# Performance work log

Measured on AMD Instinct MI355X. Metric: run time of the kernel, lower is better.

Reference implementation:

```python
import jax, jax.numpy as jnp
import numpy as np

EPS = 1e-6
B, T, E, H = 2, 512, 1024, 256
NUM_BLOCK = 12


def normalize(x):
    # RMS-style normalization over the feature dim (no learned affine)
    return x * jax.lax.rsqrt(jnp.mean(x * x, axis=-1, keepdims=True) + EPS)


def bar_quadratic_causal(a, b):
    # y_i = (1/i) * sum_{j<=i} relu(a_i + b_j)   (causal prefix mean of pairwise relation)
    # a, b: [B, T, H]
    Tn = a.shape[1]
    pair = jax.nn.relu(a[:, :, None, :] + b[:, None, :, :])  # [B, T(i), T(j), H]
    mask = jnp.tril(jnp.ones((Tn, Tn), dtype=a.dtype))        # causal j<=i
    s = jnp.einsum('bijh,ij->bih', pair, mask)
    counts = jnp.arange(1, Tn + 1, dtype=a.dtype)[None, :, None]
    return s / counts


def setup_inputs() -> dict:
    key = jax.random.key(0)
    k0, k1, k2, k3 = jax.random.split(key, 4)
    x = jax.random.normal(k0, (B, T, E), dtype=jnp.float32)
    w1 = jax.random.normal(k1, (E, H), dtype=jnp.float32) * 0.02
    b1 = jnp.zeros((H,), dtype=jnp.float32)
    w2 = jax.random.normal(k2, (E, H), dtype=jnp.float32) * 0.02
    b2 = jnp.zeros((H,), dtype=jnp.float32)
    w3 = jax.random.normal(k3, (H, E), dtype=jnp.float32) * (0.02 / np.sqrt(NUM_BLOCK))
    b3 = jnp.zeros((E,), dtype=jnp.float32)
    return {"x": x, "w1": w1, "b1": b1, "w2": w2, "b2": b2, "w3": w3, "b3": b3}


def reference(x, w1, b1, w2, b2, w3, b3):
    r = normalize(x)
    a = r @ w1 + b1
    b = r @ w2 + b2
    # PreNorm == 'approx': normalize a and b separately
    a = normalize(a)
    b = normalize(b)
    r = bar_quadratic_causal(a, b)
    # PostNorm == 'yes'
    r = normalize(r)
    r = r @ w3 + b3
    return x + r
```

## Files before the change

### kernel.cpp

```cpp
#include <hip/hip_runtime.h>

#define EPSF 1e-6f
#define Bsz 2
#define Tn  512
#define En  1024
#define Hn  256
#define Mtot (Bsz * Tn)
typedef unsigned short us_t;
typedef unsigned int   u32_t;

typedef __attribute__((ext_vector_type(8))) __fp16 f16x8;
typedef __attribute__((ext_vector_type(2))) __fp16 h2_t;
typedef __attribute__((ext_vector_type(8))) short  short8;
typedef __attribute__((ext_vector_type(4))) float  f32x4;
#define MFMA16(a, b, c) __builtin_amdgcn_mfma_f32_16x16x32_f16((a), (b), (c), 0, 0, 0)

__device__ __forceinline__ us_t f2h(float f) {
  __fp16 h = (__fp16)f;
  return __builtin_bit_cast(us_t, h);
}
__device__ __forceinline__ float h2f(us_t u) {
  return (float)__builtin_bit_cast(__fp16, u);
}
__device__ __forceinline__ uint2 pack4h(float a, float b, float c, float d) {
  uint2 r;
  r.x = (u32_t)f2h(a) | ((u32_t)f2h(b) << 16);
  r.y = (u32_t)f2h(c) | ((u32_t)f2h(d) << 16);
  return r;
}
__device__ __forceinline__ float block_reduce_sum_256(float v, float* smem) {
  #pragma unroll
  for (int off = 32; off > 0; off >>= 1) v += __shfl_down(v, off, 64);
  const int wave = threadIdx.x >> 6;
  if ((threadIdx.x & 63) == 0) smem[wave] = v;
  __syncthreads();
  float s = smem[0] + smem[1] + smem[2] + smem[3];
  __syncthreads();
  return s;
}

__global__ __launch_bounds__(256) void k_prep(
    const float* __restrict__ x,
    const float* __restrict__ w1, const float* __restrict__ w2,
    const float* __restrict__ w3,
    us_t* __restrict__ xb, float* __restrict__ rs,
    us_t* __restrict__ w1t, us_t* __restrict__ w2t, us_t* __restrict__ w3t)
{
  const int b = blockIdx.x, t = threadIdx.x;

  if (b < 256) {
    const int wid = t >> 6, lane = t & 63;
    const int q   = b >> 3;
    const int mt  = (b & 7) + 8 * (q & 7);
    const int row = 16 * mt + 4 * (q >> 3) + wid;
    const float4* xp = (const float4*)(x + (size_t)row * En);
    float4 v[4];
    #pragma unroll
    for (int i = 0; i < 4; ++i) v[i] = xp[lane + 64 * i];
    float ss = 0.f;
    #pragma unroll
    for (int i = 0; i < 4; ++i)
      ss += v[i].x*v[i].x + v[i].y*v[i].y + v[i].z*v[i].z + v[i].w*v[i].w;
    #pragma unroll
    for (int off = 32; off > 0; off >>= 1) ss += __shfl_xor(ss, off, 64);
    if (lane == 0) rs[row] = rsqrtf(ss * (1.0f / En) + EPSF);
    uint2* xo = (uint2*)(xb + (size_t)row * En);
    #pragma unroll
    for (int i = 0; i < 4; ++i)
      xo[lane + 64 * i] = pack4h(v[i].x, v[i].y, v[i].z, v[i].w);
    return;
  }

  __shared__ float ts[32][33];
  const int i = b - 256;
  const float* src; us_t* dst; int R, C, tr, tc;
  if (i < 256)      { src = w1; dst = w1t; R = 1024; C = 256;  tr = i >> 3;  tc = i & 7; }
  else if (i < 512) { int k = i - 256; src = w2; dst = w2t; R = 1024; C = 256; tr = k >> 3; tc = k & 7; }
  else              { int k = i - 512; src = w3; dst = w3t; R = 256; C = 1024; tr = k >> 5; tc = k & 31; }

  const int r = t >> 3, c4 = (t & 7) * 4;
  float4 v = *(const float4*)(src + (size_t)(tr * 32 + r) * C + tc * 32 + c4);
  ts[r][c4 + 0] = v.x; ts[r][c4 + 1] = v.y; ts[r][c4 + 2] = v.z; ts[r][c4 + 3] = v.w;
  __syncthreads();
  float o0 = ts[c4 + 0][r], o1 = ts[c4 + 1][r], o2 = ts[c4 + 2][r], o3 = ts[c4 + 3][r];
  *(uint2*)(dst + (size_t)(tc * 32 + r) * R + tr * 32 + c4) = pack4h(o0, o1, o2, o3);
}

__global__ __launch_bounds__(256, 4) void k_gemm(
    const us_t* __restrict__ xb,
    const us_t* __restrict__ w1t, const us_t* __restrict__ w2t,
    float* __restrict__ Praw)
{
  const int blk = blockIdx.x;
  const int mt = blk & 63, nt = blk >> 6;
  const int m0 = mt * 16, n0 = nt * 32;
  const int wid = threadIdx.x >> 6, lane = threadIdx.x & 63;
  const int lg = lane >> 4, lr = lane & 15;
  const int k0 = wid * 256;

  const us_t* ap = xb + (size_t)(m0 + lr) * En + k0 + lg * 8;
  const us_t* bbase = (n0 < Hn) ? (w1t + (size_t)n0 * En)
                                : (w2t + (size_t)(n0 - Hn) * En);
  const us_t* bp0 = bbase + (size_t)lr * En + k0 + lg * 8;
  const us_t* bp1 = bp0 + (size_t)16 * En;

  f16x8 a[8], b0[8], b1[8];
  #pragma unroll
  for (int s = 0; s < 8; ++s) a[s]  = *(const f16x8*)(ap  + s * 32);
  #pragma unroll
  for (int s = 0; s < 8; ++s) b0[s] = *(const f16x8*)(bp0 + s * 32);
  #pragma unroll
  for (int s = 0; s < 8; ++s) b1[s] = *(const f16x8*)(bp1 + s * 32);

  f32x4 acc0 = {0.f,0.f,0.f,0.f}, acc1 = acc0;
  #pragma unroll
  for (int s = 0; s < 8; ++s) {
    acc0 = MFMA16(a[s], b0[s], acc0);
    acc1 = MFMA16(a[s], b1[s], acc1);
  }

  __shared__ float cmb[4][16][32];
  #pragma unroll
  for (int i = 0; i < 4; ++i) {
    cmb[wid][lg * 4 + i][lr]      = acc0[i];
    cmb[wid][lg * 4 + i][16 + lr] = acc1[i];
  }
  __syncthreads();

  #pragma unroll
  for (int e = 0; e < 2; ++e) {
    const int idx = threadIdx.x + e * 256;
    const int row = idx >> 5, col = idx & 31;
    float s = cmb[0][row][col] + cmb[1][row][col]
            + cmb[2][row][col] + cmb[3][row][col];
    Praw[(size_t)(m0 + row) * 512 + n0 + col] = s;
  }
}

__global__ __launch_bounds__(256) void k_norm(
    const float* __restrict__ Praw, const float* __restrict__ rs,
    const float* __restrict__ b1, const float* __restrict__ b2,
    us_t* __restrict__ A, us_t* __restrict__ BmT)
{
  const int blk = blockIdx.x, t = threadIdx.x;
  const int wid = t >> 6, lane = t & 63;
  const int h0 = lane * 4;

  if (blk < 256) {
    const int mt = blk & 63, sub = blk >> 6;
    const int r  = 16 * mt + 4 * sub + wid;
    float4 d = *(const float4*)(Praw + (size_t)r * 512 + h0);
    const float s0 = rs[r];
    float4 bv = *(const float4*)(b1 + h0);
    float vx = d.x * s0 + bv.x, vy = d.y * s0 + bv.y;
    float vz = d.z * s0 + bv.z, vw = d.w * s0 + bv.w;

    float ss = vx*vx + vy*vy + vz*vz + vw*vw;
    #pragma unroll
    for (int o2 = 32; o2 > 0; o2 >>= 1) ss += __shfl_xor(ss, o2, 64);
    const float sc = rsqrtf(ss * (1.0f / Hn) + EPSF);
    *(uint2*)(A + (size_t)r * Hn + h0) = pack4h(vx*sc, vy*sc, vz*sc, vw*sc);
    return;
  }

  __shared__ us_t ls[4][256];
  const int m  = blk - 256;
  const int mt = m & 63, sub = m >> 6;
  const int r0 = 16 * mt + 4 * sub;
  const int r  = r0 + wid;

  float4 d = *(const float4*)(Praw + (size_t)r * 512 + Hn + h0);
  const float s0 = rs[r];
  float4 bv = *(const float4*)(b2 + h0);
  float vx = d.x * s0 + bv.x, vy = d.y * s0 + bv.y;
  float vz = d.z * s0 + bv.z, vw = d.w * s0 + bv.w;

  float ss = vx*vx + vy*vy + vz*vz + vw*vw;
  #pragma unroll
  for (int o2 = 32; o2 > 0; o2 >>= 1) ss += __shfl_xor(ss, o2, 64);
  const float sc = rsqrtf(ss * (1.0f / Hn) + EPSF);

  *(uint2*)&ls[wid][h0] = pack4h(vx*sc, vy*sc, vz*sc, vw*sc);
  __syncthreads();

  const int h = t;
  u32_t w0  = (u32_t)ls[0][h] | ((u32_t)ls[1][h] << 16);
  u32_t w1v = (u32_t)ls[2][h] | ((u32_t)ls[3][h] << 16);
  const int bb   = r0 >> 9;
  const int tcol = r0 & 511;
  *(uint2*)(BmT + (size_t)bb * Hn * Tn + (size_t)h * Tn + tcol) = make_uint2(w0, w1v);
}

#define JCHB 32
__global__ __launch_bounds__(256) void k_bar(
    const us_t* __restrict__ A, const us_t* __restrict__ BmT,
    us_t* __restrict__ Yb)
{
  const int raw = blockIdx.x;
  const int sel = (raw < 256) ? raw : (511 - raw);
  const int bb  = raw >> 8;
  const int i0  = sel * 2;
  const int h   = threadIdx.x;
  const size_t baseA = (size_t)bb * Tn * Hn;
  const us_t* __restrict__ bt = BmT + (size_t)bb * Hn * Tn + (size_t)h * Tn;

  const __fp16 a0h = __builtin_bit_cast(__fp16, A[baseA + (size_t)i0 * Hn + h]);
  const __fp16 a1h = __builtin_bit_cast(__fp16, A[baseA + (size_t)(i0 + 1) * Hn + h]);
  const float av0 = (float)a0h;
  const float av1 = (float)a1h;
  h2_t z2;  z2[0]  = (__fp16)0.f; z2[1]  = (__fp16)0.f;
  h2_t a02; a02[0] = a0h;         a02[1] = a0h;
  h2_t a12; a12[0] = a1h;         a12[1] = a1h;
  float sum0 = 0.f, sum1 = 0.f;

  const int nfull = i0 & ~(JCHB - 1);
  short8 c0[4], c1[4];

  #define LOADC(dst, jj) { _Pragma("unroll") \
    for (int q = 0; q < 4; ++q) dst[q] = *(const short8*)(bt + (jj) + q * 8); }
  #define PROCP(buf) { _Pragma("unroll") \
    for (int q = 0; q < 4; ++q) { \
      const h2_t* ph = (const h2_t*)&buf[q]; \
      h2_t p0 = z2, p1 = z2; \
      _Pragma("unroll") \
      for (int w2i = 0; w2i < 4; ++w2i) { \
        h2_t bv2 = ph[w2i]; \
        p0 += __builtin_elementwise_max(a02 + bv2, z2); \
        p1 += __builtin_elementwise_max(a12 + bv2, z2); \
      } \
      sum0 += (float)p0[0] + (float)p0[1]; \
      sum1 += (float)p1[0] + (float)p1[1]; } }

  if (nfull > 0) {
    LOADC(c0, 0);
    int j = 0;
    while (true) {
      const bool m1 = (j + JCHB     < nfull);
      const bool m2 = (j + 2 * JCHB < nfull);
      if (m1) LOADC(c1, j + JCHB);
      PROCP(c0);
      j += JCHB;
      if (!m1) break;
      if (m2) LOADC(c0, j + JCHB);
      PROCP(c1);
      j += JCHB;
      if (!m2) break;
    }
  }
  {
    short8 ct[4];
    LOADC(ct, nfull);
    const int lim = i0 - nfull;
    #pragma unroll
    for (int q = 0; q < 4; ++q)
      #pragma unroll
      for (int e = 0; e < 8; ++e) {
        const int jl = q * 8 + e;
        float bv = h2f((us_t)ct[q][e]);
        sum0 += (jl <= lim)     ? fmaxf(av0 + bv, 0.f) : 0.f;
        sum1 += (jl <= lim + 1) ? fmaxf(av1 + bv, 0.f) : 0.f;
      }
  }
  #undef LOADC
  #undef PROCP

  __shared__ float red[4];
  {
    float ss = block_reduce_sum_256(sum0 * sum0, red);
    float c  = (float)(i0 + 1);
    float sc = rsqrtf(ss * (1.0f / Hn) + EPSF * c * c);
    Yb[baseA + (size_t)i0 * Hn + h] = f2h(sum0 * sc);
  }
  {
    float ss = block_reduce_sum_256(sum1 * sum1, red);
    float c  = (float)(i0 + 2);
    float sc = rsqrtf(ss * (1.0f / Hn) + EPSF * c * c);
    Yb[baseA + (size_t)(i0 + 1) * Hn + h] = f2h(sum1 * sc);
  }
}

__global__ __launch_bounds__(256, 4) void k_out(
    const us_t* __restrict__ Yb, const us_t* __restrict__ w3t,
    const float* __restrict__ x, const float* __restrict__ b3,
    float* __restrict__ out)
{
  const int wid = threadIdx.x >> 6, lane = threadIdx.x & 63;
  const int wg = blockIdx.x * 4 + wid;
  const int nt = wg & 63, mt = wg >> 6;
  const int m0 = mt * 16, n0 = nt * 16;
  const int lg = lane >> 4, lr = lane & 15;

  const us_t* ap = Yb  + (size_t)(m0 + lr) * Hn + lg * 8;
  const us_t* bp = w3t + (size_t)(n0 + lr) * Hn + lg * 8;

  f16x8 a[8], b[8];
  #pragma unroll
  for (int s = 0; s < 8; ++s) a[s] = *(const f16x8*)(ap + s * 32);
  #pragma unroll
  for (int s = 0; s < 8; ++s) b[s] = *(const f16x8*)(bp + s * 32);

  f32x4 acc = {0.f,0.f,0.f,0.f};
  #pragma unroll
  for (int s = 0; s < 8; ++s) acc = MFMA16(a[s], b[s], acc);

  const int row = m0 + lg * 4;
  const int c = n0 + lr;
  const float bv = b3[c];
  #pragma unroll
  for (int i = 0; i < 4; ++i) {
    const size_t o = (size_t)(row + i) * En + c;
    out[o] = x[o] + acc[i] + bv;
  }
}

extern "C" void kernel_launch(void* const* d_in, const int* in_sizes, int n_in,
                              void* d_out, int out_size, void* d_ws, size_t ws_size,
                              hipStream_t stream) {
  const float* x  = (const float*)d_in[0];
  const float* w1 = (const float*)d_in[1];
  const float* b1 = (const float*)d_in[2];
  const float* w2 = (const float*)d_in[3];
  const float* b2 = (const float*)d_in[4];
  const float* w3 = (const float*)d_in[5];
  const float* b3 = (const float*)d_in[6];
  float* out = (float*)d_out;

  char* q = (char*)d_ws;
  float* Praw = (float*)q;  q += (size_t)Mtot * 512 * 4;
  us_t* xb    = (us_t*)q;   q += (size_t)Mtot * En * 2;
  us_t* w1t   = (us_t*)q;   q += (size_t)Hn * En * 2;
  us_t* w2t   = (us_t*)q;   q += (size_t)Hn * En * 2;
  us_t* w3t   = (us_t*)q;   q += (size_t)En * Hn * 2;
  us_t* A     = (us_t*)q;   q += (size_t)Mtot * Hn * 2;
  us_t* BmT   = (us_t*)q;   q += (size_t)Mtot * Hn * 2;
  us_t* Yb    = (us_t*)q;   q += (size_t)Mtot * Hn * 2;
  float* rs   = (float*)q;  q += (size_t)Mtot * 4;

  k_prep<<<1024, 256, 0, stream>>>(x, w1, w2, w3, xb, rs, w1t, w2t, w3t);
  k_gemm<<<1024, 256, 0, stream>>>(xb, w1t, w2t, Praw);
  k_norm<<<512,  256, 0, stream>>>(Praw, rs, b1, b2, A, BmT);
  k_bar <<<512,  256, 0, stream>>>(A, BmT, Yb);
  k_out <<<1024, 256, 0, stream>>>(Yb, w3t, x, b3, out);
}
```

Before: 46.67 us.

## Fuse input RMS-norm into GEMM prologue and row-norm into last-block epilogue

Each GEMM block now computes the RMS scale of its 16 input rows and stages the normalized fp16 rows in shared memory, so the separate xb conversion buffer and the rs array are gone. The k_norm launch is removed. A per-row-tile atomic ticket lets the last of the 16 column blocks for that tile normalize both projection outputs and write A and the transposed B. This cuts one launch and the intermediate traffic, at the cost of every block re-reading x from global memory, the larger shared-memory footprint lowering occupancy, and a serialized epilogue in the last block.

```diff
diff --git a/kernel.cpp b/kernel.cpp
--- a/kernel.cpp
+++ b/kernel.cpp
@@ -39,44 +39,20 @@
   return s;
 }
 
-__global__ __launch_bounds__(256) void k_prep(
-    const float* __restrict__ x,
+__global__ __launch_bounds__(256) void k_tr(
     const float* __restrict__ w1, const float* __restrict__ w2,
     const float* __restrict__ w3,
-    us_t* __restrict__ xb, float* __restrict__ rs,
-    us_t* __restrict__ w1t, us_t* __restrict__ w2t, us_t* __restrict__ w3t)
+    us_t* __restrict__ w1t, us_t* __restrict__ w2t, us_t* __restrict__ w3t,
+    int* __restrict__ ticket)
 {
   const int b = blockIdx.x, t = threadIdx.x;
-
-  if (b < 256) {
-    const int wid = t >> 6, lane = t & 63;
-    const int q   = b >> 3;
-    const int mt  = (b & 7) + 8 * (q & 7);
-    const int row = 16 * mt + 4 * (q >> 3) + wid;
-    const float4* xp = (const float4*)(x + (size_t)row * En);
-    float4 v[4];
-    #pragma unroll
-    for (int i = 0; i < 4; ++i) v[i] = xp[lane + 64 * i];
-    float ss = 0.f;
-    #pragma unroll
-    for (int i = 0; i < 4; ++i)
-      ss += v[i].x*v[i].x + v[i].y*v[i].y + v[i].z*v[i].z + v[i].w*v[i].w;
-    #pragma unroll
-    for (int off = 32; off > 0; off >>= 1) ss += __shfl_xor(ss, off, 64);
-    if (lane == 0) rs[row] = rsqrtf(ss * (1.0f / En) + EPSF);
-    uint2* xo = (uint2*)(xb + (size_t)row * En);
-    #pragma unroll
-    for (int i = 0; i < 4; ++i)
-      xo[lane + 64 * i] = pack4h(v[i].x, v[i].y, v[i].z, v[i].w);
-    return;
-  }
+  if (b == 0 && t < 64) ticket[t] = 0;
 
   __shared__ float ts[32][33];
-  const int i = b - 256;
   const float* src; us_t* dst; int R, C, tr, tc;
-  if (i < 256)      { src = w1; dst = w1t; R = 1024; C = 256;  tr = i >> 3;  tc = i & 7; }
-  else if (i < 512) { int k = i - 256; src = w2; dst = w2t; R = 1024; C = 256; tr = k >> 3; tc = k & 7; }
-  else              { int k = i - 512; src = w3; dst = w3t; R = 256; C = 1024; tr = k >> 5; tc = k & 31; }
+  if (b < 256)      { src = w1; dst = w1t; R = 1024; C = 256;  tr = b >> 3;  tc = b & 7; }
+  else if (b < 512) { int k = b - 256; src = w2; dst = w2t; R = 1024; C = 256; tr = k >> 3; tc = k & 7; }
+  else              { int k = b - 512; src = w3; dst = w3t; R = 256; C = 1024; tr = k >> 5; tc = k & 31; }
 
   const int r = t >> 3, c4 = (t & 7) * 4;
   float4 v = *(const float4*)(src + (size_t)(tr * 32 + r) * C + tc * 32 + c4);
@@ -87,108 +63,148 @@
 }
 
 __global__ __launch_bounds__(256, 4) void k_gemm(
-    const us_t* __restrict__ xb,
+    const float* __restrict__ x,
     const us_t* __restrict__ w1t, const us_t* __restrict__ w2t,
-    float* __restrict__ Praw)
+    const float* __restrict__ b1, const float* __restrict__ b2,
+    float* __restrict__ Praw, int* __restrict__ ticket,
+    us_t* __restrict__ A, us_t* __restrict__ BmT)
 {
+  union SM {
+    us_t xs[16][1032];
+    struct { float cmb[4][16][32]; us_t ls[16][256]; } ep;
+  };
+  __shared__ SM sm;
+  __shared__ int winf;
+
   const int blk = blockIdx.x;
   const int mt = blk & 63, nt = blk >> 6;
   const int m0 = mt * 16, n0 = nt * 32;
-  const int wid = threadIdx.x >> 6, lane = threadIdx.x & 63;
+  const int t = threadIdx.x;
+
+  {
+    const int r  = t >> 4;
+    const int cs = t & 15;
+    const float* xr = x + (size_t)(m0 + r) * En;
+    float ss = 0.f;
+    #pragma unroll
+    for (int i = 0; i < 16; ++i) {
+      float4 v = *(const float4*)(xr + i * 64 + cs * 4);
+      ss += v.x*v.x + v.y*v.y + v.z*v.z + v.w*v.w;
+    }
+    #pragma unroll
+    for (int o = 1; o < 16; o <<= 1) ss += __shfl_xor(ss, o, 64);
+    const float sc = rsqrtf(ss * (1.0f / En) + EPSF);
+    #pragma unroll
+    for (int i = 0; i < 16; ++i) {
+      float4 v = *(const float4*)(xr + i * 64 + cs * 4);
+      *(uint2*)&sm.xs[r][i * 64 + cs * 4] =
+          pack4h(v.x * sc, v.y * sc, v.z * sc, v.w * sc);
+    }
+  }
+  __syncthreads();
+
+  const int wid = t >> 6, lane = t & 63;
   const int lg = lane >> 4, lr = lane & 15;
   const int k0 = wid * 256;
 
-  const us_t* ap = xb + (size_t)(m0 + lr) * En + k0 + lg * 8;
   const us_t* bbase = (n0 < Hn) ? (w1t + (size_t)n0 * En)
                                 : (w2t + (size_t)(n0 - Hn) * En);
   const us_t* bp0 = bbase + (size_t)lr * En + k0 + lg * 8;
   const us_t* bp1 = bp0 + (size_t)16 * En;
 
-  f16x8 a[8], b0[8], b1[8];
-  #pragma unroll
-  for (int s = 0; s < 8; ++s) a[s]  = *(const f16x8*)(ap  + s * 32);
-  #pragma unroll
-  for (int s = 0; s < 8; ++s) b0[s] = *(const f16x8*)(bp0 + s * 32);
-  #pragma unroll
-  for (int s = 0; s < 8; ++s) b1[s] = *(const f16x8*)(bp1 + s * 32);
+  f16x8 wf0[8], wf1[8];
+  #pragma unroll
+  for (int s = 0; s < 8; ++s) wf0[s] = *(const f16x8*)(bp0 + s * 32);
+  #pragma unroll
+  for (int s = 0; s < 8; ++s) wf1[s] = *(const f16x8*)(bp1 + s * 32);
 
   f32x4 acc0 = {0.f,0.f,0.f,0.f}, acc1 = acc0;
   #pragma unroll
   for (int s = 0; s < 8; ++s) {
-    acc0 = MFMA16(a[s], b0[s], acc0);
-    acc1 = MFMA16(a[s], b1[s], acc1);
-  }
-
-  __shared__ float cmb[4][16][32];
+    f16x8 a = *(const f16x8*)&sm.xs[lr][k0 + lg * 8 + s * 32];
+    acc0 = MFMA16(a, wf0[s], acc0);
+    acc1 = MFMA16(a, wf1[s], acc1);
+  }
+  __syncthreads();
+
   #pragma unroll
   for (int i = 0; i < 4; ++i) {
-    cmb[wid][lg * 4 + i][lr]      = acc0[i];
-    cmb[wid][lg * 4 + i][16 + lr] = acc1[i];
-  }
-  __syncthreads();
-
+    sm.ep.cmb[wid][lg * 4 + i][lr]      = acc0[i];
+    sm.ep.cmb[wid][lg * 4 + i][16 + lr] = acc1[i];
+  }
+  __syncthreads();
   #pragma unroll
   for (int e = 0; e < 2; ++e) {
-    const int idx = threadIdx.x + e * 256;
+    const int idx = t + e * 256;
     const int row = idx >> 5, col = idx & 31;
-    float s = cmb[0][row][col] + cmb[1][row][col]
-            + cmb[2][row][col] + cmb[3][row][col];
+    float s = sm.ep.cmb[0][row][col] + sm.ep.cmb[1][row][col]
+            + sm.ep.cmb[2][row][col] + sm.ep.cmb[3][row][col];
     Praw[(size_t)(m0 + row) * 512 + n0 + col] = s;
   }
-}
-
-__global__ __launch_bounds__(256) void k_norm(
-    const float* __restrict__ Praw, const float* __restrict__ rs,
-    const float* __restrict__ b1, const float* __restrict__ b2,
-    us_t* __restrict__ A, us_t* __restrict__ BmT)
-{
-  const int blk = blockIdx.x, t = threadIdx.x;
-  const int wid = t >> 6, lane = t & 63;
-  const int h0 = lane * 4;
-
-  if (blk < 256) {
-    const int mt = blk & 63, sub = blk >> 6;
-    const int r  = 16 * mt + 4 * sub + wid;
-    float4 d = *(const float4*)(Praw + (size_t)r * 512 + h0);
-    const float s0 = rs[r];
-    float4 bv = *(const float4*)(b1 + h0);
-    float vx = d.x * s0 + bv.x, vy = d.y * s0 + bv.y;
-    float vz = d.z * s0 + bv.z, vw = d.w * s0 + bv.w;
-
-    float ss = vx*vx + vy*vy + vz*vz + vw*vw;
-    #pragma unroll
-    for (int o2 = 32; o2 > 0; o2 >>= 1) ss += __shfl_xor(ss, o2, 64);
+
+  __threadfence();
+  __syncthreads();
+  if (t == 0) winf = (atomicAdd(&ticket[mt], 1) == 15);
+  __syncthreads();
+  if (!winf) return;
+
+  const int r  = t >> 4;
+  const int cs = t & 15;
+  const float* pr = Praw + (size_t)(m0 + r) * 512;
+
+  {
+    float v[16]; float ss = 0.f;
+    #pragma unroll
+    for (int q = 0; q < 4; ++q) {
+      float4 d  = *(const float4*)(pr + cs * 16 + q * 4);
+      float4 bv = *(const float4*)(b1 + cs * 16 + q * 4);
+      v[q*4+0] = d.x + bv.x; v[q*4+1] = d.y + bv.y;
+      v[q*4+2] = d.z + bv.z; v[q*4+3] = d.w + bv.w;
+    }
+    #pragma unroll
+    for (int k = 0; k < 16; ++k) ss += v[k] * v[k];
+    #pragma unroll
+    for (int o = 1; o < 16; o <<= 1) ss += __shfl_xor(ss, o, 64);
     const float sc = rsqrtf(ss * (1.0f / Hn) + EPSF);
-    *(uint2*)(A + (size_t)r * Hn + h0) = pack4h(vx*sc, vy*sc, vz*sc, vw*sc);
-    return;
-  }
-
-  __shared__ us_t ls[4][256];
-  const int m  = blk - 256;
-  const int mt = m & 63, sub = m >> 6;
-  const int r0 = 16 * mt + 4 * sub;
-  const int r  = r0 + wid;
-
-  float4 d = *(const float4*)(Praw + (size_t)r * 512 + Hn + h0);
-  const float s0 = rs[r];
-  float4 bv = *(const float4*)(b2 + h0);
-  float vx = d.x * s0 + bv.x, vy = d.y * s0 + bv.y;
-  float vz = d.z * s0 + bv.z, vw = d.w * s0 + bv.w;
-
-  float ss = vx*vx + vy*vy + vz*vz + vw*vw;
-  #pragma unroll
-  for (int o2 = 32; o2 > 0; o2 >>= 1) ss += __shfl_xor(ss, o2, 64);
-  const float sc = rsqrtf(ss * (1.0f / Hn) + EPSF);
-
-  *(uint2*)&ls[wid][h0] = pack4h(vx*sc, vy*sc, vz*sc, vw*sc);
-  __syncthreads();
-
-  const int h = t;
-  u32_t w0  = (u32_t)ls[0][h] | ((u32_t)ls[1][h] << 16);
-  u32_t w1v = (u32_t)ls[2][h] | ((u32_t)ls[3][h] << 16);
-  const int bb   = r0 >> 9;
-  const int tcol = r0 & 511;
-  *(uint2*)(BmT + (size_t)bb * Hn * Tn + (size_t)h * Tn + tcol) = make_uint2(w0, w1v);
+    us_t* ao = A + (size_t)(m0 + r) * Hn + cs * 16;
+    #pragma unroll
+    for (int q = 0; q < 4; ++q)
+      ((uint2*)ao)[q] = pack4h(v[q*4]*sc, v[q*4+1]*sc, v[q*4+2]*sc, v[q*4+3]*sc);
+  }
+  {
+    float v[16]; float ss = 0.f;
+    #pragma unroll
+    for (int q = 0; q < 4; ++q) {
+      float4 d  = *(const float4*)(pr + Hn + cs * 16 + q * 4);
+      float4 bv = *(const float4*)(b2 + cs * 16 + q * 4);
+      v[q*4+0] = d.x + bv.x; v[q*4+1] = d.y + bv.y;
+      v[q*4+2] = d.z + bv.z; v[q*4+3] = d.w + bv.w;
+    }
+    #pragma unroll
+    for (int k = 0; k < 16; ++k) ss += v[k] * v[k];
+    #pragma unroll
+    for (int o = 1; o < 16; o <<= 1) ss += __shfl_xor(ss, o, 64);
+    const float sc = rsqrtf(ss * (1.0f / Hn) + EPSF);
+    #pragma unroll
+    for (int q = 0; q < 4; ++q)
+      *(uint2*)&sm.ep.ls[r][cs * 16 + q * 4] =
+          pack4h(v[q*4]*sc, v[q*4+1]*sc, v[q*4+2]*sc, v[q*4+3]*sc);
+  }
+  __syncthreads();
+  {
+    const int h = t;
+    us_t col[16];
+    #pragma unroll
+    for (int j = 0; j < 16; ++j) col[j] = sm.ep.ls[j][h];
+    u32_t w[8];
+    #pragma unroll
+    for (int k = 0; k < 8; ++k)
+      w[k] = (u32_t)col[2*k] | ((u32_t)col[2*k+1] << 16);
+    const int bb = m0 >> 9, tcol = m0 & 511;
+    us_t* bt = BmT + (size_t)bb * Hn * Tn + (size_t)h * Tn + tcol;
+    ((uint4*)bt)[0] = make_uint4(w[0], w[1], w[2], w[3]);
+    ((uint4*)bt)[1] = make_uint4(w[4], w[5], w[6], w[7]);
+  }
 }
 
 #define JCHB 32
@@ -327,18 +343,16 @@
 
   char* q = (char*)d_ws;
   float* Praw = (float*)q;  q += (size_t)Mtot * 512 * 4;
-  us_t* xb    = (us_t*)q;   q += (size_t)Mtot * En * 2;
   us_t* w1t   = (us_t*)q;   q += (size_t)Hn * En * 2;
   us_t* w2t   = (us_t*)q;   q += (size_t)Hn * En * 2;
   us_t* w3t   = (us_t*)q;   q += (size_t)En * Hn * 2;
   us_t* A     = (us_t*)q;   q += (size_t)Mtot * Hn * 2;
   us_t* BmT   = (us_t*)q;   q += (size_t)Mtot * Hn * 2;
   us_t* Yb    = (us_t*)q;   q += (size_t)Mtot * Hn * 2;
-  float* rs   = (float*)q;  q += (size_t)Mtot * 4;
-
-  k_prep<<<1024, 256, 0, stream>>>(x, w1, w2, w3, xb, rs, w1t, w2t, w3t);
-  k_gemm<<<1024, 256, 0, stream>>>(xb, w1t, w2t, Praw);
-  k_norm<<<512,  256, 0, stream>>>(Praw, rs, b1, b2, A, BmT);
+  int* ticket = (int*)q;    q += 64 * sizeof(int);
+
+  k_tr  <<<768,  256, 0, stream>>>(w1, w2, w3, w1t, w2t, w3t, ticket);
+  k_gemm<<<1024, 256, 0, stream>>>(x, w1t, w2t, b1, b2, Praw, ticket, A, BmT);
   k_bar <<<512,  256, 0, stream>>>(A, BmT, Yb);
   k_out <<<1024, 256, 0, stream>>>(Yb, w3t, x, b3, out);
 }
```

Result: slower. 129.4 us (+177.3%).

## Split work across more threads in gemm, bar and output kernels

Applied to the files above, without the earlier changes.

The causal-bar kernel now runs 512 threads per block. Each half processes alternating 32-column j-chunks, and the two partial sums are combined in shared memory before the row normalization. The input GEMM tile shrinks from 32 to 16 output columns, which doubles the grid and uses fewer registers per block. The output GEMM splits K across wave pairs, with a shared-memory reduction. The aim is more parallelism and latency hiding, at the cost of extra shared-memory traffic and barriers.

```diff
diff --git a/kernel.cpp b/kernel.cpp
--- a/kernel.cpp
+++ b/kernel.cpp
@@ -28,13 +28,14 @@
   r.y = (u32_t)f2h(c) | ((u32_t)f2h(d) << 16);
   return r;
 }
-__device__ __forceinline__ float block_reduce_sum_256(float v, float* smem) {
+__device__ __forceinline__ float block_reduce_sum_512(float v, float* smem) {
   #pragma unroll
   for (int off = 32; off > 0; off >>= 1) v += __shfl_down(v, off, 64);
   const int wave = threadIdx.x >> 6;
   if ((threadIdx.x & 63) == 0) smem[wave] = v;
   __syncthreads();
-  float s = smem[0] + smem[1] + smem[2] + smem[3];
+  float s = smem[0] + smem[1] + smem[2] + smem[3]
+          + smem[4] + smem[5] + smem[6] + smem[7];
   __syncthreads();
   return s;
 }
@@ -86,14 +87,14 @@
   *(uint2*)(dst + (size_t)(tc * 32 + r) * R + tr * 32 + c4) = pack4h(o0, o1, o2, o3);
 }
 
-__global__ __launch_bounds__(256, 4) void k_gemm(
+__global__ __launch_bounds__(256, 8) void k_gemm(
     const us_t* __restrict__ xb,
     const us_t* __restrict__ w1t, const us_t* __restrict__ w2t,
     float* __restrict__ Praw)
 {
   const int blk = blockIdx.x;
   const int mt = blk & 63, nt = blk >> 6;
-  const int m0 = mt * 16, n0 = nt * 32;
+  const int m0 = mt * 16, n0 = nt * 16;
   const int wid = threadIdx.x >> 6, lane = threadIdx.x & 63;
   const int lg = lane >> 4, lr = lane & 15;
   const int k0 = wid * 256;
@@ -101,40 +102,26 @@
   const us_t* ap = xb + (size_t)(m0 + lr) * En + k0 + lg * 8;
   const us_t* bbase = (n0 < Hn) ? (w1t + (size_t)n0 * En)
                                 : (w2t + (size_t)(n0 - Hn) * En);
-  const us_t* bp0 = bbase + (size_t)lr * En + k0 + lg * 8;
-  const us_t* bp1 = bp0 + (size_t)16 * En;
-
-  f16x8 a[8], b0[8], b1[8];
-  #pragma unroll
-  for (int s = 0; s < 8; ++s) a[s]  = *(const f16x8*)(ap  + s * 32);
-  #pragma unroll
-  for (int s = 0; s < 8; ++s) b0[s] = *(const f16x8*)(bp0 + s * 32);
-  #pragma unroll
-  for (int s = 0; s < 8; ++s) b1[s] = *(const f16x8*)(bp1 + s * 32);
-
-  f32x4 acc0 = {0.f,0.f,0.f,0.f}, acc1 = acc0;
+  const us_t* bp = bbase + (size_t)lr * En + k0 + lg * 8;
+
+  f32x4 acc = {0.f,0.f,0.f,0.f};
   #pragma unroll
   for (int s = 0; s < 8; ++s) {
-    acc0 = MFMA16(a[s], b0[s], acc0);
-    acc1 = MFMA16(a[s], b1[s], acc1);
-  }
-
-  __shared__ float cmb[4][16][32];
-  #pragma unroll
-  for (int i = 0; i < 4; ++i) {
-    cmb[wid][lg * 4 + i][lr]      = acc0[i];
-    cmb[wid][lg * 4 + i][16 + lr] = acc1[i];
-  }
-  __syncthreads();
-
-  #pragma unroll
-  for (int e = 0; e < 2; ++e) {
-    const int idx = threadIdx.x + e * 256;
-    const int row = idx >> 5, col = idx & 31;
-    float s = cmb[0][row][col] + cmb[1][row][col]
-            + cmb[2][row][col] + cmb[3][row][col];
-    Praw[(size_t)(m0 + row) * 512 + n0 + col] = s;
-  }
+    f16x8 a = *(const f16x8*)(ap + s * 32);
+    f16x8 b = *(const f16x8*)(bp + s * 32);
+    acc = MFMA16(a, b, acc);
+  }
+
+  __shared__ float cmb[4][16][16];
+  #pragma unroll
+  for (int i = 0; i < 4; ++i)
+    cmb[wid][lg * 4 + i][lr] = acc[i];
+  __syncthreads();
+
+  const int row = threadIdx.x >> 4, col = threadIdx.x & 15;
+  float s = cmb[0][row][col] + cmb[1][row][col]
+          + cmb[2][row][col] + cmb[3][row][col];
+  Praw[(size_t)(m0 + row) * 512 + n0 + col] = s;
 }
 
 __global__ __launch_bounds__(256) void k_norm(
@@ -192,7 +179,7 @@
 }
 
 #define JCHB 32
-__global__ __launch_bounds__(256) void k_bar(
+__global__ __launch_bounds__(512) void k_bar(
     const us_t* __restrict__ A, const us_t* __restrict__ BmT,
     us_t* __restrict__ Yb)
 {
@@ -200,7 +187,8 @@
   const int sel = (raw < 256) ? raw : (511 - raw);
   const int bb  = raw >> 8;
   const int i0  = sel * 2;
-  const int h   = threadIdx.x;
+  const int t   = threadIdx.x;
+  const int h   = t & 255, jh = t >> 8;
   const size_t baseA = (size_t)bb * Tn * Hn;
   const us_t* __restrict__ bt = BmT + (size_t)bb * Hn * Tn + (size_t)h * Tn;
 
@@ -213,8 +201,8 @@
   h2_t a12; a12[0] = a1h;         a12[1] = a1h;
   float sum0 = 0.f, sum1 = 0.f;
 
-  const int nfull = i0 & ~(JCHB - 1);
-  short8 c0[4], c1[4];
+  const int nch = i0 >> 5;
+  short8 c0v[4], c1v[4];
 
   #define LOADC(dst, jj) { _Pragma("unroll") \
     for (int q = 0; q < 4; ++q) dst[q] = *(const short8*)(bt + (jj) + q * 8); }
@@ -231,26 +219,28 @@
       sum0 += (float)p0[0] + (float)p0[1]; \
       sum1 += (float)p1[0] + (float)p1[1]; } }
 
-  if (nfull > 0) {
-    LOADC(c0, 0);
-    int j = 0;
+  int ch = jh;
+  if (ch < nch) {
+    LOADC(c0v, ch * JCHB);
     while (true) {
-      const bool m1 = (j + JCHB     < nfull);
-      const bool m2 = (j + 2 * JCHB < nfull);
-      if (m1) LOADC(c1, j + JCHB);
-      PROCP(c0);
-      j += JCHB;
-      if (!m1) break;
-      if (m2) LOADC(c0, j + JCHB);
-      PROCP(c1);
-      j += JCHB;
-      if (!m2) break;
+      int nx = ch + 2;
+      bool more = (nx < nch);
+      if (more) LOADC(c1v, nx * JCHB);
+      PROCP(c0v);
+      ch = nx;
+      if (!more) break;
+      nx = ch + 2;
+      more = (nx < nch);
+      if (more) LOADC(c0v, nx * JCHB);
+      PROCP(c1v);
+      ch = nx;
+      if (!more) break;
     }
   }
-  {
+  if (jh == (nch & 1)) {
     short8 ct[4];
-    LOADC(ct, nfull);
-    const int lim = i0 - nfull;
+    LOADC(ct, nch * JCHB);
+    const int lim = i0 - nch * JCHB;
     #pragma unroll
     for (int q = 0; q < 4; ++q)
       #pragma unroll
@@ -264,52 +254,68 @@
   #undef LOADC
   #undef PROCP
 
-  __shared__ float red[4];
-  {
-    float ss = block_reduce_sum_256(sum0 * sum0, red);
-    float c  = (float)(i0 + 1);
-    float sc = rsqrtf(ss * (1.0f / Hn) + EPSF * c * c);
-    Yb[baseA + (size_t)i0 * Hn + h] = f2h(sum0 * sc);
-  }
-  {
-    float ss = block_reduce_sum_256(sum1 * sum1, red);
-    float c  = (float)(i0 + 2);
-    float sc = rsqrtf(ss * (1.0f / Hn) + EPSF * c * c);
-    Yb[baseA + (size_t)(i0 + 1) * Hn + h] = f2h(sum1 * sc);
-  }
-}
-
-__global__ __launch_bounds__(256, 4) void k_out(
+  __shared__ float part0[2][256], part1[2][256];
+  __shared__ float red[8];
+  part0[jh][h] = sum0;
+  part1[jh][h] = sum1;
+  __syncthreads();
+
+  const float tot0 = part0[0][h] + part0[1][h];
+  const float tot1 = part1[0][h] + part1[1][h];
+
+  float ss0 = block_reduce_sum_512((jh == 0) ? tot0 * tot0 : 0.f, red);
+  float ss1 = block_reduce_sum_512((jh == 0) ? tot1 * tot1 : 0.f, red);
+
+  if (jh == 0) {
+    float cA = (float)(i0 + 1);
+    float scA = rsqrtf(ss0 * (1.0f / Hn) + EPSF * cA * cA);
+    Yb[baseA + (size_t)i0 * Hn + h] = f2h(tot0 * scA);
+    float cB = (float)(i0 + 2);
+    float scB = rsqrtf(ss1 * (1.0f / Hn) + EPSF * cB * cB);
+    Yb[baseA + (size_t)(i0 + 1) * Hn + h] = f2h(tot1 * scB);
+  }
+}
+
+__global__ __launch_bounds__(256, 8) void k_out(
     const us_t* __restrict__ Yb, const us_t* __restrict__ w3t,
     const float* __restrict__ x, const float* __restrict__ b3,
     float* __restrict__ out)
 {
   const int wid = threadIdx.x >> 6, lane = threadIdx.x & 63;
-  const int wg = blockIdx.x * 4 + wid;
-  const int nt = wg & 63, mt = wg >> 6;
+  const int tl = wid >> 1, ks = wid & 1;
+  const int wt = blockIdx.x * 2 + tl;
+  const int mt = wt >> 6, nt = wt & 63;
   const int m0 = mt * 16, n0 = nt * 16;
   const int lg = lane >> 4, lr = lane & 15;
-
-  const us_t* ap = Yb  + (size_t)(m0 + lr) * Hn + lg * 8;
-  const us_t* bp = w3t + (size_t)(n0 + lr) * Hn + lg * 8;
-
-  f16x8 a[8], b[8];
-  #pragma unroll
-  for (int s = 0; s < 8; ++s) a[s] = *(const f16x8*)(ap + s * 32);
-  #pragma unroll
-  for (int s = 0; s < 8; ++s) b[s] = *(const f16x8*)(bp + s * 32);
+  const int k0 = ks * 128;
+
+  const us_t* ap = Yb  + (size_t)(m0 + lr) * Hn + k0 + lg * 8;
+  const us_t* bp = w3t + (size_t)(n0 + lr) * Hn + k0 + lg * 8;
 
   f32x4 acc = {0.f,0.f,0.f,0.f};
   #pragma unroll
-  for (int s = 0; s < 8; ++s) acc = MFMA16(a[s], b[s], acc);
-
-  const int row = m0 + lg * 4;
-  const int c = n0 + lr;
-  const float bv = b3[c];
-  #pragma unroll
-  for (int i = 0; i < 4; ++i) {
-    const size_t o = (size_t)(row + i) * En + c;
-    out[o] = x[o] + acc[i] + bv;
+  for (int s = 0; s < 4; ++s) {
+    f16x8 a = *(const f16x8*)(ap + s * 32);
+    f16x8 b = *(const f16x8*)(bp + s * 32);
+    acc = MFMA16(a, b, acc);
+  }
+
+  __shared__ float cmb[4][16][16];
+  #pragma unroll
+  for (int i = 0; i < 4; ++i)
+    cmb[wid][lg * 4 + i][lr] = acc[i];
+  __syncthreads();
+
+  const int row = (threadIdx.x >> 4) & 15, col = threadIdx.x & 15;
+  #pragma unroll
+  for (int e = 0; e < 2; ++e) {
+    if ((threadIdx.x >> 8) == 0) {
+      const int wt_e = blockIdx.x * 2 + e;
+      const int m0e = (wt_e >> 6) * 16, n0e = (wt_e & 63) * 16;
+      float s = cmb[e * 2][row][col] + cmb[e * 2 + 1][row][col];
+      const size_t o = (size_t)(m0e + row) * En + n0e + col;
+      out[o] = x[o] + s + b3[n0e + col];
+    }
   }
 }
 
@@ -337,8 +343,8 @@
   float* rs   = (float*)q;  q += (size_t)Mtot * 4;
 
   k_prep<<<1024, 256, 0, stream>>>(x, w1, w2, w3, xb, rs, w1t, w2t, w3t);
-  k_gemm<<<1024, 256, 0, stream>>>(xb, w1t, w2t, Praw);
+  k_gemm<<<2048, 256, 0, stream>>>(xb, w1t, w2t, Praw);
   k_norm<<<512,  256, 0, stream>>>(Praw, rs, b1, b2, A, BmT);
-  k_bar <<<512,  256, 0, stream>>>(A, BmT, Yb);
-  k_out <<<1024, 256, 0, stream>>>(Yb, w3t, x, b3, out);
-}
+  k_bar <<<512,  512, 0, stream>>>(A, BmT, Yb);
+  k_out <<<2048, 256, 0, stream>>>(Yb, w3t, x, b3, out);
+}
```

Result: slower. 51.31 us (+9.9%).
